# Kernel optimization log

Measured on AMD Instinct MI355X. Metric: run time of the kernel, lower is better.

The kernel has to match this reference:

```python
import jax, jax.numpy as jnp
import numpy as np

VOCAB = 100000
EMBED = 128
BATCH = 16384
POS = 10
NEG = 50


def setup_inputs() -> dict:
    key = jax.random.key(0)
    k1, k2, k3, k4, k5 = jax.random.split(key, 5)
    input_labels = jax.random.randint(k1, (BATCH,), 0, VOCAB)
    pos_labels = jax.random.randint(k2, (BATCH, POS), 0, VOCAB)
    neg_labels = jax.random.randint(k3, (BATCH, NEG), 0, VOCAB)
    in_embed = jax.random.normal(k4, (VOCAB, EMBED), dtype=jnp.float32)
    out_embed = jax.random.normal(k5, (VOCAB, EMBED), dtype=jnp.float32)
    return {
        "input_labels": input_labels,
        "pos_labels": pos_labels,
        "neg_labels": neg_labels,
        "in_embed": in_embed,
        "out_embed": out_embed,
    }


def reference(input_labels, pos_labels, neg_labels, in_embed, out_embed):
    # gathers
    center = in_embed[input_labels]          # [B, D]
    pos = out_embed[pos_labels]              # [B, P, D]
    neg = out_embed[neg_labels]              # [B, N, D]
    # batched dot products: [B, P], [B, N]
    pos_dot = jnp.einsum("bpd,bd->bp", pos, center)
    neg_dot = jnp.einsum("bnd,bd->bn", neg, center)
    log_pos = jax.nn.log_sigmoid(pos_dot).sum(axis=1)  # [B]
    log_neg = jax.nn.log_sigmoid(neg_dot).sum(axis=1)  # [B]
    loss = log_pos - log_neg
    return -loss
```

## Files before the change

kernel.cpp:

```cpp
#include <hip/hip_runtime.h>
#include <hip/hip_bf16.h>
#include <math.h>

#define VOCAB 100000
#define EMBED 128
#define BATCH 16384
#define NPOS 10
#define NNEG 50
#define NLAB (NPOS + NNEG)


__device__ __forceinline__ float fast_log_sigmoid(float x) {
    const float e = __expf(-fabsf(x));
    return fminf(x, 0.0f) - __logf(1.0f + e);
}

__device__ __forceinline__ float dot4(float4 a, float4 b) {
    return fmaf(a.x, b.x, fmaf(a.y, b.y, fmaf(a.z, b.z, a.w * b.w)));
}

__device__ __forceinline__ unsigned bf16rne(float f) {
    unsigned u = __float_as_uint(f);
    return (u + 0x7fffu + ((u >> 16) & 1u)) >> 16;
}
__device__ __forceinline__ unsigned pack2(float lo, float hi) {
    return bf16rne(lo) | (bf16rne(hi) << 16);
}

__device__ __forceinline__ float dot8(float4 x, float4 y, uint4 v) {
    const float f0 = __uint_as_float(v.x << 16);
    const float f1 = __uint_as_float(v.x & 0xffff0000u);
    const float f2 = __uint_as_float(v.y << 16);
    const float f3 = __uint_as_float(v.y & 0xffff0000u);
    const float f4 = __uint_as_float(v.z << 16);
    const float f5 = __uint_as_float(v.z & 0xffff0000u);
    const float f6 = __uint_as_float(v.w << 16);
    const float f7 = __uint_as_float(v.w & 0xffff0000u);
    const float a = fmaf(x.x, f0, fmaf(x.y, f1, fmaf(x.z, f2, x.w * f3)));
    const float b = fmaf(y.x, f4, fmaf(y.y, f5, fmaf(y.z, f6, y.w * f7)));
    return a + b;
}

__global__ __launch_bounds__(256) void cvt_bf16_kernel(
    const float* __restrict__ src, unsigned* __restrict__ dst, int n8)
{
    int i = blockIdx.x * 256 + threadIdx.x;
    const int stride = gridDim.x * 256;
    const float4* __restrict__ s4 = reinterpret_cast<const float4*>(src);
    uint4* __restrict__ d4 = reinterpret_cast<uint4*>(dst);
    for (; i < n8; i += stride) {
        const float4 a = s4[2 * i];
        const float4 b = s4[2 * i + 1];
        uint4 o;
        o.x = pack2(a.x, a.y);
        o.y = pack2(a.z, a.w);
        o.z = pack2(b.x, b.y);
        o.w = pack2(b.z, b.w);
        d4[i] = o;
    }
}

__global__ __launch_bounds__(256) void skipgram_loss_bf16_kernel(
    const int* __restrict__ input_labels,
    const int* __restrict__ pos_labels,
    const int* __restrict__ neg_labels,
    const float* __restrict__ in_embed,
    const unsigned* __restrict__ out_bf,
    float* __restrict__ out)
{
    const int wave = threadIdx.x >> 6;
    const int lane = threadIdx.x & 63;
    const int b = blockIdx.x * 4 + wave;
    const int g = lane >> 3;
    const int t = lane & 7;

    const float* __restrict__ crow = in_embed + (unsigned)input_labels[b] * EMBED;
    const float4 ca = *reinterpret_cast<const float4*>(crow + t * 8);
    const float4 cb = *reinterpret_cast<const float4*>(crow + t * 8 + 4);
    const float4 cc = *reinterpret_cast<const float4*>(crow + 64 + t * 8);
    const float4 cd = *reinterpret_cast<const float4*>(crow + 64 + t * 8 + 4);

    int lab;
    if (lane < NPOS)       lab = pos_labels[b * NPOS + lane];
    else if (lane < NLAB)  lab = neg_labels[b * NNEG + (lane - NPOS)];
    else                   lab = 0;

    unsigned roff[8];
    #pragma unroll
    for (int p = 0; p < 8; ++p)
        roff[p] = (unsigned)__shfl(lab, p * 8 + g) * 64u + (unsigned)(t * 4);

    uint4 u0 = *reinterpret_cast<const uint4*>(out_bf + roff[0]);
    uint4 u1 = *reinterpret_cast<const uint4*>(out_bf + roff[0] + 32);

    float total = 0.0f;
    #pragma unroll
    for (int p = 0; p < 8; ++p) {
        uint4 n0, n1;
        if (p < 7) {
            n0 = *reinterpret_cast<const uint4*>(out_bf + roff[p + 1]);
            n1 = *reinterpret_cast<const uint4*>(out_bf + roff[p + 1] + 32);
        }

        float acc = dot8(ca, cb, u0) + dot8(cc, cd, u1);

        acc += __shfl_xor(acc, 1);
        acc += __shfl_xor(acc, 2);
        acc += __shfl_xor(acc, 4);

        const int li = p * 8 + g;
        const float wl = (li < NLAB) ? ((li < NPOS) ? -1.0f : 1.0f) : 0.0f;
        total += (t == 0) ? wl * fast_log_sigmoid(acc) : 0.0f;

        if (p < 7) { u0 = n0; u1 = n1; }
    }

    total += __shfl_xor(total, 8);
    total += __shfl_xor(total, 16);
    total += __shfl_xor(total, 32);

    if (lane == 0) out[b] = total;
}

__global__ __launch_bounds__(256) void skipgram_loss_f32_kernel(
    const int* __restrict__ input_labels,
    const int* __restrict__ pos_labels,
    const int* __restrict__ neg_labels,
    const float* __restrict__ in_embed,
    const float* __restrict__ out_embed,
    float* __restrict__ out)
{
    const int wave = threadIdx.x >> 6;
    const int lane = threadIdx.x & 63;
    const int b = blockIdx.x * 4 + wave;
    const int g = lane >> 3;
    const int t = lane & 7;

    const unsigned coff = (unsigned)input_labels[b] * EMBED + (unsigned)(t * 4);
    const float4 c0 = *reinterpret_cast<const float4*>(in_embed + coff);
    const float4 c1 = *reinterpret_cast<const float4*>(in_embed + coff + 32);
    const float4 c2 = *reinterpret_cast<const float4*>(in_embed + coff + 64);
    const float4 c3 = *reinterpret_cast<const float4*>(in_embed + coff + 96);

    int lab;
    if (lane < NPOS)       lab = pos_labels[b * NPOS + lane];
    else if (lane < NLAB)  lab = neg_labels[b * NNEG + (lane - NPOS)];
    else                   lab = 0;

    unsigned roff[8];
    #pragma unroll
    for (int p = 0; p < 8; ++p)
        roff[p] = (unsigned)__shfl(lab, p * 8 + g) * EMBED + (unsigned)(t * 4);

    float4 u0 = *reinterpret_cast<const float4*>(out_embed + roff[0]);
    float4 u1 = *reinterpret_cast<const float4*>(out_embed + roff[0] + 32);
    float4 u2 = *reinterpret_cast<const float4*>(out_embed + roff[0] + 64);
    float4 u3 = *reinterpret_cast<const float4*>(out_embed + roff[0] + 96);

    float total = 0.0f;
    #pragma unroll
    for (int p = 0; p < 8; ++p) {
        float4 n0, n1, n2, n3;
        if (p < 7) {
            n0 = *reinterpret_cast<const float4*>(out_embed + roff[p + 1]);
            n1 = *reinterpret_cast<const float4*>(out_embed + roff[p + 1] + 32);
            n2 = *reinterpret_cast<const float4*>(out_embed + roff[p + 1] + 64);
            n3 = *reinterpret_cast<const float4*>(out_embed + roff[p + 1] + 96);
        }
        float acc = dot4(c0, u0) + dot4(c1, u1) + dot4(c2, u2) + dot4(c3, u3);
        acc += __shfl_xor(acc, 1);
        acc += __shfl_xor(acc, 2);
        acc += __shfl_xor(acc, 4);
        const int li = p * 8 + g;
        const float wl = (li < NLAB) ? ((li < NPOS) ? -1.0f : 1.0f) : 0.0f;
        total += (t == 0) ? wl * fast_log_sigmoid(acc) : 0.0f;
        if (p < 7) { u0 = n0; u1 = n1; u2 = n2; u3 = n3; }
    }

    total += __shfl_xor(total, 8);
    total += __shfl_xor(total, 16);
    total += __shfl_xor(total, 32);

    if (lane == 0) out[b] = total;
}

extern "C" void kernel_launch(void* const* d_in, const int* in_sizes, int n_in,
                              void* d_out, int out_size, void* d_ws, size_t ws_size,
                              hipStream_t stream) {
    const int*   input_labels = (const int*)d_in[0];
    const int*   pos_labels   = (const int*)d_in[1];
    const int*   neg_labels   = (const int*)d_in[2];
    const float* in_embed     = (const float*)d_in[3];
    const float* out_embed    = (const float*)d_in[4];
    float*       out          = (float*)d_out;

    const size_t need = (size_t)VOCAB * EMBED * sizeof(unsigned short);
    const int blocks = BATCH / 4;

    if (ws_size >= need) {
        unsigned* out_bf = (unsigned*)d_ws;
        const int n8 = VOCAB * EMBED / 8;
        cvt_bf16_kernel<<<2048, 256, 0, stream>>>(out_embed, out_bf, n8);
        skipgram_loss_bf16_kernel<<<blocks, 256, 0, stream>>>(
            input_labels, pos_labels, neg_labels, in_embed, out_bf, out);
    } else {
        skipgram_loss_f32_kernel<<<blocks, 256, 0, stream>>>(
            input_labels, pos_labels, neg_labels, in_embed, out_embed, out);
    }
}
```

Measured before the change: 50.73 us.

## Bucket gather work by vocabulary slice to improve cache locality

Adds a bucketing pass that sorts every (batch, label) pair into eight vocabulary slices. The main kernel then processes one slice per block group, so the gathered bf16 rows from a slice can stay resident in cache. Center embeddings are also pre-converted to bf16 in their own buffer, and per-element loss terms are accumulated into the output with float atomics after zeroing it. This costs extra kernel launches, index traffic and heavy atomic contention on the output. The f32 fallback path is removed, so small workspaces compute nothing beyond the bf16 path.

```diff
diff --git a/kernel.cpp b/kernel.cpp
--- a/kernel.cpp
+++ b/kernel.cpp
@@ -7,18 +7,25 @@
 #define BATCH 16384
 #define NPOS 10
 #define NNEG 50
-#define NLAB (NPOS + NNEG)
-
+#define NLAB 60
+#define NSLICE 8
+#define SLICE_ROWS (VOCAB / NSLICE)
+#define CAP 131072
+
+#define WS_TABLE   0u
+#define WS_CBUF    25600000u
+#define WS_BSLOT   (WS_CBUF + 4194304u)
+#define WS_LAB     (WS_BSLOT + 4194304u)
+#define WS_COUNTS  (WS_LAB + 4194304u)
+#define WS_NEED    (WS_COUNTS + 64u)
 
 __device__ __forceinline__ float fast_log_sigmoid(float x) {
     const float e = __expf(-fabsf(x));
     return fminf(x, 0.0f) - __logf(1.0f + e);
 }
-
 __device__ __forceinline__ float dot4(float4 a, float4 b) {
     return fmaf(a.x, b.x, fmaf(a.y, b.y, fmaf(a.z, b.z, a.w * b.w)));
 }
-
 __device__ __forceinline__ unsigned bf16rne(float f) {
     unsigned u = __float_as_uint(f);
     return (u + 0x7fffu + ((u >> 16) & 1u)) >> 16;
@@ -26,19 +33,36 @@
 __device__ __forceinline__ unsigned pack2(float lo, float hi) {
     return bf16rne(lo) | (bf16rne(hi) << 16);
 }
-
+__device__ __forceinline__ float bl(unsigned u) { return __uint_as_float(u << 16); }
+__device__ __forceinline__ float bh(unsigned u) { return __uint_as_float(u & 0xffff0000u); }
+__device__ __forceinline__ float dot8bb(uint4 a, uint4 b) {
+    float acc =      bl(a.x) * bl(b.x);
+    acc = fmaf(bh(a.x), bh(b.x), acc);
+    acc = fmaf(bl(a.y), bl(b.y), acc);
+    acc = fmaf(bh(a.y), bh(b.y), acc);
+    acc = fmaf(bl(a.z), bl(b.z), acc);
+    acc = fmaf(bh(a.z), bh(b.z), acc);
+    acc = fmaf(bl(a.w), bl(b.w), acc);
+    acc = fmaf(bh(a.w), bh(b.w), acc);
+    return acc;
+}
 __device__ __forceinline__ float dot8(float4 x, float4 y, uint4 v) {
-    const float f0 = __uint_as_float(v.x << 16);
-    const float f1 = __uint_as_float(v.x & 0xffff0000u);
-    const float f2 = __uint_as_float(v.y << 16);
-    const float f3 = __uint_as_float(v.y & 0xffff0000u);
-    const float f4 = __uint_as_float(v.z << 16);
-    const float f5 = __uint_as_float(v.z & 0xffff0000u);
-    const float f6 = __uint_as_float(v.w << 16);
-    const float f7 = __uint_as_float(v.w & 0xffff0000u);
-    const float a = fmaf(x.x, f0, fmaf(x.y, f1, fmaf(x.z, f2, x.w * f3)));
-    const float b = fmaf(y.x, f4, fmaf(y.y, f5, fmaf(y.z, f6, y.w * f7)));
-    return a + b;
+    float acc =      x.x * bl(v.x);
+    acc = fmaf(x.y, bh(v.x), acc);
+    acc = fmaf(x.z, bl(v.y), acc);
+    acc = fmaf(x.w, bh(v.y), acc);
+    acc = fmaf(y.x, bl(v.z), acc);
+    acc = fmaf(y.y, bh(v.z), acc);
+    acc = fmaf(y.z, bl(v.w), acc);
+    acc = fmaf(y.w, bh(v.w), acc);
+    return acc;
+}
+
+__global__ __launch_bounds__(256) void zero_kernel(float* __restrict__ out,
+                                                   unsigned* __restrict__ counts) {
+    const int i = blockIdx.x * 256 + threadIdx.x;
+    if (i < BATCH) out[i] = 0.0f;
+    if (i < NSLICE) counts[i] = 0u;
 }
 
 __global__ __launch_bounds__(256) void cvt_bf16_kernel(
@@ -60,6 +84,102 @@
     }
 }
 
+__global__ __launch_bounds__(256) void cbuf_kernel(
+    const int* __restrict__ input_labels, const float* __restrict__ in_embed,
+    unsigned* __restrict__ cbuf)
+{
+    const int gid = blockIdx.x * 256 + threadIdx.x;
+    const int b = gid >> 5, part = gid & 31;
+    const float4 v = *reinterpret_cast<const float4*>(
+        in_embed + (unsigned)input_labels[b] * EMBED + part * 4);
+    uint2 o;
+    o.x = pack2(v.x, v.y);
+    o.y = pack2(v.z, v.w);
+    *reinterpret_cast<uint2*>(cbuf + b * 64 + part * 2) = o;
+}
+
+__global__ __launch_bounds__(256) void bucket_kernel(
+    const int* __restrict__ pos_labels, const int* __restrict__ neg_labels,
+    unsigned* __restrict__ ebslot, unsigned* __restrict__ elab,
+    unsigned* __restrict__ counts)
+{
+    __shared__ unsigned cnt[NSLICE], base[NSLICE], cur[NSLICE];
+    const int tid = threadIdx.x;
+    const int b0 = blockIdx.x * 64;
+    if (tid < NSLICE) { cnt[tid] = 0u; cur[tid] = 0u; }
+    __syncthreads();
+    for (int e = tid; e < 64 * NLAB; e += 256) {
+        const int q = e / NLAB, slot = e - q * NLAB;
+        const int b = b0 + q;
+        const int label = (slot < NPOS) ? pos_labels[b * NPOS + slot]
+                                        : neg_labels[b * NNEG + (slot - NPOS)];
+        atomicAdd(&cnt[label / SLICE_ROWS], 1u);
+    }
+    __syncthreads();
+    if (tid < NSLICE) base[tid] = atomicAdd(&counts[tid], cnt[tid]);
+    __syncthreads();
+    for (int e = tid; e < 64 * NLAB; e += 256) {
+        const int q = e / NLAB, slot = e - q * NLAB;
+        const int b = b0 + q;
+        const int label = (slot < NPOS) ? pos_labels[b * NPOS + slot]
+                                        : neg_labels[b * NNEG + (slot - NPOS)];
+        const int s = label / SLICE_ROWS;
+        const unsigned pos = base[s] + atomicAdd(&cur[s], 1u);
+        if (pos < CAP) {
+            ebslot[s * CAP + pos] = ((unsigned)b << 6) | (unsigned)slot;
+            elab[s * CAP + pos]   = (unsigned)label;
+        }
+    }
+}
+
+__global__ __launch_bounds__(256) void main_kernel(
+    const unsigned* __restrict__ ebslot, const unsigned* __restrict__ elab,
+    const unsigned* __restrict__ counts, const unsigned* __restrict__ table,
+    const unsigned* __restrict__ cbuf, float* __restrict__ out)
+{
+    const int s = blockIdx.x & 7;
+    const int j = blockIdx.x >> 3;
+    const int wave = threadIdx.x >> 6;
+    const int lane = threadIdx.x & 63;
+    const int g = lane >> 3, t = lane & 7;
+
+    unsigned count = counts[s];
+    if (count > CAP) count = CAP;
+    const unsigned* __restrict__ bsl = ebslot + s * CAP;
+    const unsigned* __restrict__ lb  = elab + s * CAP;
+
+    for (unsigned i0 = (unsigned)j * 32u; i0 < count; i0 += 256u * 32u) {
+        const unsigned wbase = i0 + (unsigned)wave * 8u;
+        unsigned my_bslot = 0u, my_lab = 0u;
+        const unsigned li = wbase + (unsigned)lane;
+        if (lane < 8 && li < count) { my_bslot = bsl[li]; my_lab = lb[li]; }
+        const unsigned ebs = __shfl(my_bslot, g);
+        const unsigned el  = __shfl(my_lab,  g);
+        const bool valid = (wbase + (unsigned)g) < count;
+        const int b    = (int)(ebs >> 6);
+        const int slot = (int)(ebs & 63u);
+
+        float acc = 0.0f;
+        if (valid) {
+            const unsigned co = (unsigned)b * 64u + (unsigned)(t * 4);
+            const uint4 c0 = *reinterpret_cast<const uint4*>(cbuf + co);
+            const uint4 c1 = *reinterpret_cast<const uint4*>(cbuf + co + 32);
+            const unsigned ro = el * 64u + (unsigned)(t * 4);
+            const uint4 r0 = *reinterpret_cast<const uint4*>(table + ro);
+            const uint4 r1 = *reinterpret_cast<const uint4*>(table + ro + 32);
+            acc = dot8bb(c0, r0) + dot8bb(c1, r1);
+        }
+        acc += __shfl_xor(acc, 1);
+        acc += __shfl_xor(acc, 2);
+        acc += __shfl_xor(acc, 4);
+
+        if (t == 0 && valid) {
+            const float w = (slot < NPOS) ? -1.0f : 1.0f;
+            atomicAdd(&out[b], w * fast_log_sigmoid(acc));
+        }
+    }
+}
+
 __global__ __launch_bounds__(256) void skipgram_loss_bf16_kernel(
     const int* __restrict__ input_labels,
     const int* __restrict__ pos_labels,
@@ -71,8 +191,7 @@
     const int wave = threadIdx.x >> 6;
     const int lane = threadIdx.x & 63;
     const int b = blockIdx.x * 4 + wave;
-    const int g = lane >> 3;
-    const int t = lane & 7;
+    const int g = lane >> 3, t = lane & 7;
 
     const float* __restrict__ crow = in_embed + (unsigned)input_labels[b] * EMBED;
     const float4 ca = *reinterpret_cast<const float4*>(crow + t * 8);
@@ -101,86 +220,18 @@
             n0 = *reinterpret_cast<const uint4*>(out_bf + roff[p + 1]);
             n1 = *reinterpret_cast<const uint4*>(out_bf + roff[p + 1] + 32);
         }
-
         float acc = dot8(ca, cb, u0) + dot8(cc, cd, u1);
-
         acc += __shfl_xor(acc, 1);
         acc += __shfl_xor(acc, 2);
         acc += __shfl_xor(acc, 4);
-
-        const int li = p * 8 + g;
-        const float wl = (li < NLAB) ? ((li < NPOS) ? -1.0f : 1.0f) : 0.0f;
+        const int lix = p * 8 + g;
+        const float wl = (lix < NLAB) ? ((lix < NPOS) ? -1.0f : 1.0f) : 0.0f;
         total += (t == 0) ? wl * fast_log_sigmoid(acc) : 0.0f;
-
         if (p < 7) { u0 = n0; u1 = n1; }
     }
-
     total += __shfl_xor(total, 8);
     total += __shfl_xor(total, 16);
     total += __shfl_xor(total, 32);
-
-    if (lane == 0) out[b] = total;
-}
-
-__global__ __launch_bounds__(256) void skipgram_loss_f32_kernel(
-    const int* __restrict__ input_labels,
-    const int* __restrict__ pos_labels,
-    const int* __restrict__ neg_labels,
-    const float* __restrict__ in_embed,
-    const float* __restrict__ out_embed,
-    float* __restrict__ out)
-{
-    const int wave = threadIdx.x >> 6;
-    const int lane = threadIdx.x & 63;
-    const int b = blockIdx.x * 4 + wave;
-    const int g = lane >> 3;
-    const int t = lane & 7;
-
-    const unsigned coff = (unsigned)input_labels[b] * EMBED + (unsigned)(t * 4);
-    const float4 c0 = *reinterpret_cast<const float4*>(in_embed + coff);
-    const float4 c1 = *reinterpret_cast<const float4*>(in_embed + coff + 32);
-    const float4 c2 = *reinterpret_cast<const float4*>(in_embed + coff + 64);
-    const float4 c3 = *reinterpret_cast<const float4*>(in_embed + coff + 96);
-
-    int lab;
-    if (lane < NPOS)       lab = pos_labels[b * NPOS + lane];
-    else if (lane < NLAB)  lab = neg_labels[b * NNEG + (lane - NPOS)];
-    else                   lab = 0;
-
-    unsigned roff[8];
-    #pragma unroll
-    for (int p = 0; p < 8; ++p)
-        roff[p] = (unsigned)__shfl(lab, p * 8 + g) * EMBED + (unsigned)(t * 4);
-
-    float4 u0 = *reinterpret_cast<const float4*>(out_embed + roff[0]);
-    float4 u1 = *reinterpret_cast<const float4*>(out_embed + roff[0] + 32);
-    float4 u2 = *reinterpret_cast<const float4*>(out_embed + roff[0] + 64);
-    float4 u3 = *reinterpret_cast<const float4*>(out_embed + roff[0] + 96);
-
-    float total = 0.0f;
-    #pragma unroll
-    for (int p = 0; p < 8; ++p) {
-        float4 n0, n1, n2, n3;
-        if (p < 7) {
-            n0 = *reinterpret_cast<const float4*>(out_embed + roff[p + 1]);
-            n1 = *reinterpret_cast<const float4*>(out_embed + roff[p + 1] + 32);
-            n2 = *reinterpret_cast<const float4*>(out_embed + roff[p + 1] + 64);
-            n3 = *reinterpret_cast<const float4*>(out_embed + roff[p + 1] + 96);
-        }
-        float acc = dot4(c0, u0) + dot4(c1, u1) + dot4(c2, u2) + dot4(c3, u3);
-        acc += __shfl_xor(acc, 1);
-        acc += __shfl_xor(acc, 2);
-        acc += __shfl_xor(acc, 4);
-        const int li = p * 8 + g;
-        const float wl = (li < NLAB) ? ((li < NPOS) ? -1.0f : 1.0f) : 0.0f;
-        total += (t == 0) ? wl * fast_log_sigmoid(acc) : 0.0f;
-        if (p < 7) { u0 = n0; u1 = n1; u2 = n2; u3 = n3; }
-    }
-
-    total += __shfl_xor(total, 8);
-    total += __shfl_xor(total, 16);
-    total += __shfl_xor(total, 32);
-
     if (lane == 0) out[b] = total;
 }
 
@@ -194,17 +245,26 @@
     const float* out_embed    = (const float*)d_in[4];
     float*       out          = (float*)d_out;
 
-    const size_t need = (size_t)VOCAB * EMBED * sizeof(unsigned short);
-    const int blocks = BATCH / 4;
-
-    if (ws_size >= need) {
-        unsigned* out_bf = (unsigned*)d_ws;
-        const int n8 = VOCAB * EMBED / 8;
-        cvt_bf16_kernel<<<2048, 256, 0, stream>>>(out_embed, out_bf, n8);
-        skipgram_loss_bf16_kernel<<<blocks, 256, 0, stream>>>(
-            input_labels, pos_labels, neg_labels, in_embed, out_bf, out);
-    } else {
-        skipgram_loss_f32_kernel<<<blocks, 256, 0, stream>>>(
-            input_labels, pos_labels, neg_labels, in_embed, out_embed, out);
-    }
-}
+    char* ws = (char*)d_ws;
+    const int n8 = VOCAB * EMBED / 8;
+
+    if (ws_size >= WS_NEED) {
+        unsigned* table  = (unsigned*)(ws + WS_TABLE);
+        unsigned* cbuf   = (unsigned*)(ws + WS_CBUF);
+        unsigned* ebslot = (unsigned*)(ws + WS_BSLOT);
+        unsigned* elab   = (unsigned*)(ws + WS_LAB);
+        unsigned* counts = (unsigned*)(ws + WS_COUNTS);
+
+        zero_kernel<<<(BATCH + 255) / 256, 256, 0, stream>>>(out, counts);
+        cvt_bf16_kernel<<<2048, 256, 0, stream>>>(out_embed, table, n8);
+        cbuf_kernel<<<BATCH * 32 / 256, 256, 0, stream>>>(input_labels, in_embed, cbuf);
+        bucket_kernel<<<BATCH / 64, 256, 0, stream>>>(pos_labels, neg_labels,
+                                                      ebslot, elab, counts);
+        main_kernel<<<2048, 256, 0, stream>>>(ebslot, elab, counts, table, cbuf, out);
+    } else if (ws_size >= (size_t)VOCAB * EMBED * 2) {
+        unsigned* table = (unsigned*)ws;
+        cvt_bf16_kernel<<<2048, 256, 0, stream>>>(out_embed, table, n8);
+        skipgram_loss_bf16_kernel<<<BATCH / 4, 256, 0, stream>>>(
+            input_labels, pos_labels, neg_labels, in_embed, table, out);
+    }
+}
```

New measurement: 163.9 us. 3.23x slower.
